# Kernel tuning notes

Measured on AMD Instinct MI355X. Metric: run time of the kernel, lower is better.

## Reference

```python
import jax, jax.numpy as jnp
import numpy as np

DIM = 512
HEADS = 8
HEAD_DIM = DIM // HEADS
SCALE = DIM ** (-0.5)  # source uses full dim, not head_dim
LAMBDA_COND = 1.0


def setup_inputs() -> dict:
    key = jax.random.key(0)
    ks = jax.random.split(key, 16)
    b, n, m_a, m_s = 4, 2048, 2048, 256
    s = 0.02
    inp = {
        "x": jax.random.normal(ks[0], (b, n, DIM), jnp.float32),
        "audio_context": jax.random.normal(ks[1], (b, m_a, DIM), jnp.float32),
        "singer_context": jax.random.normal(ks[2], (b, m_s, DIM), jnp.float32),
        "Wq": jax.random.normal(ks[3], (DIM, DIM), jnp.float32) * s,
        "bq": jnp.zeros((DIM,), jnp.float32),
        "Wka": jax.random.normal(ks[4], (DIM, DIM), jnp.float32) * s,
        "bka": jnp.zeros((DIM,), jnp.float32),
        "Wva": jax.random.normal(ks[5], (DIM, DIM), jnp.float32) * s,
        "bva": jnp.zeros((DIM,), jnp.float32),
        "Wks": jax.random.normal(ks[6], (DIM, DIM), jnp.float32) * s,
        "bks": jnp.zeros((DIM,), jnp.float32),
        "Wvs": jax.random.normal(ks[7], (DIM, DIM), jnp.float32) * s,
        "bvs": jnp.zeros((DIM,), jnp.float32),
        "Wp": jax.random.normal(ks[8], (DIM, DIM), jnp.float32) * s,
        "bp": jnp.zeros((DIM,), jnp.float32),
    }
    return inp


def _heads(t):
    b, n, c = t.shape
    return t.reshape(b, n, HEADS, HEAD_DIM).transpose(0, 2, 1, 3)  # (b,h,n,d)


def _attend(q, ctx, Wk, bk, Wv, bv):
    k = _heads(ctx @ Wk.T + bk)
    v = _heads(ctx @ Wv.T + bv)
    attn = jax.nn.softmax(jnp.einsum("bhnd,bhmd->bhnm", q, k) * SCALE, axis=-1)
    o = jnp.einsum("bhnm,bhmd->bhnd", attn, v)
    b, h, n, d = o.shape
    return o.transpose(0, 2, 1, 3).reshape(b, n, h * d)


def reference(x, audio_context, singer_context, Wq, bq, Wka, bka, Wva, bva,
              Wks, bks, Wvs, bvs, Wp, bp):
    q = _heads(x @ Wq.T + bq)
    x_audio = _attend(q, audio_context, Wka, bka, Wva, bva)
    x_singer = _attend(q, singer_context, Wks, bks, Wvs, bvs)
    out = x_audio + LAMBDA_COND * x_singer
    return out @ Wp.T + bp
```

## Files before the change

### kernel.cpp

```cpp
#include <hip/hip_runtime.h>

#define DIM 512
#define NQ 2048
#define MA 2048
#define MS 256
#define QSCALE 0.06375864651f

typedef __attribute__((ext_vector_type(8))) short bf16x8;
typedef __attribute__((ext_vector_type(4))) float f32x4;
typedef __attribute__((ext_vector_type(16))) float f32x16;

__device__ __forceinline__ ushort f2b(float f) {
    uint u = __float_as_uint(f);
    u = (u + 0x7fffu + ((u >> 16) & 1u)) >> 16;
    return (ushort)u;
}

__device__ __forceinline__ void gload16(const ushort* g, ushort* l) {
    __builtin_amdgcn_global_load_lds(
        (const __attribute__((address_space(1))) void*)g,
        (__attribute__((address_space(3))) void*)l, 16, 0, 0);
}

__global__ __launch_bounds__(256) void cast_all(const float* __restrict__ w0,
                                                const float* __restrict__ w1,
                                                const float* __restrict__ w2,
                                                const float* __restrict__ w3,
                                                const float* __restrict__ w4,
                                                const float* __restrict__ w5,
                                                const float* __restrict__ x,
                                                const float* __restrict__ ac,
                                                const float* __restrict__ scx,
                                                ushort* __restrict__ dst) {
    int i = blockIdx.x * 256 + threadIdx.x;
    const float* s;
    int o;
    if (i < 393216) {
        int w = i >> 16;
        s = w < 3 ? (w == 0 ? w0 : (w == 1 ? w1 : w2))
                  : (w == 3 ? w3 : (w == 4 ? w4 : w5));
        o = i & 65535;
    } else if (i < 1441792) { s = x;   o = i - 393216; }
    else if (i < 2490368)   { s = ac;  o = i - 1441792; }
    else                    { s = scx; o = i - 2490368; }
    float4 v = ((const float4*)s)[o];
    ushort4 u;
    u.x = f2b(v.x); u.y = f2b(v.y); u.z = f2b(v.z); u.w = f2b(v.w);
    ((ushort4*)dst)[i] = u;
}

struct GD {
    const ushort* A; const ushort* B; const float* bias; void* out;
    long sB, sO;
    int N, bx, by, blk0, biasrow, scaleq, outf32, pad;
};

__global__ __launch_bounds__(256) void gemm_fused(GD d0, GD d1, GD d2, GD d3, GD d4) {
    __shared__ ushort At[128 * 32];
    __shared__ ushort Bt[128 * 32];
    GD d = d0;
    int bid = blockIdx.x;
    if (bid >= d1.blk0) d = d1;
    if (bid >= d2.blk0) d = d2;
    if (bid >= d3.blk0) d = d3;
    if (bid >= d4.blk0) d = d4;
    int local = bid - d.blk0;
    int x = local % d.bx;
    int rem = local / d.bx;
    int y = rem % d.by;
    int z = rem / d.by;

    int t = threadIdx.x;
    int wv = t >> 6, ln = t & 63, l = ln & 15, g = ln >> 4;
    int wrow = wv & 1, wcol = wv >> 1;
    int row0 = x * 128, col0 = y * 128;
    int srow = t >> 2;
    int slot = (t & 3) * 8;
    int sko = ((t ^ srow) & 3) * 8;
    int kc8 = ((g ^ (l & 3)) & 3) * 8;
    const ushort* Ab = d.A;
    const ushort* Bb = d.B + (size_t)z * d.sB;
    int N = d.N;

    f32x4 acc[4][4];
#pragma unroll
    for (int i = 0; i < 4; i++)
#pragma unroll
        for (int j = 0; j < 4; j++) acc[i][j] = (f32x4){0, 0, 0, 0};

    for (int k0 = 0; k0 < 512; k0 += 32) {
        __syncthreads();
#pragma unroll
        for (int c = 0; c < 2; c++) {
            gload16(Ab + (size_t)(row0 + srow + 64 * c) * 512 + k0 + sko,
                    At + (srow + 64 * c) * 32 + slot);
            gload16(Bb + (size_t)(col0 + srow + 64 * c) * 512 + k0 + sko,
                    Bt + (srow + 64 * c) * 32 + slot);
        }
        __syncthreads();
        bf16x8 ar[4], br[4];
#pragma unroll
        for (int i = 0; i < 4; i++)
            ar[i] = *(const bf16x8*)(At + (wrow * 64 + i * 16 + l) * 32 + kc8);
#pragma unroll
        for (int j = 0; j < 4; j++)
            br[j] = *(const bf16x8*)(Bt + (wcol * 64 + j * 16 + l) * 32 + kc8);
#pragma unroll
        for (int i = 0; i < 4; i++)
#pragma unroll
            for (int j = 0; j < 4; j++)
                acc[i][j] = __builtin_amdgcn_mfma_f32_16x16x32_bf16(ar[i], br[j], acc[i][j], 0, 0, 0);
    }
#pragma unroll
    for (int i = 0; i < 4; i++) {
#pragma unroll
        for (int j = 0; j < 4; j++) {
            int row = row0 + wrow * 64 + i * 16 + g * 4;
            int col = col0 + wcol * 64 + j * 16 + l;
#pragma unroll
            for (int r = 0; r < 4; r++) {
                float bv = d.biasrow ? d.bias[row + r] : d.bias[col];
                float o = acc[i][j][r] + bv;
                if (d.scaleq) o *= QSCALE;
                if (d.outf32)
                    ((float*)d.out + (size_t)z * d.sO)[(size_t)(row + r) * N + col] = o;
                else
                    ((ushort*)d.out + (size_t)z * d.sO)[(size_t)(row + r) * N + col] = f2b(o);
            }
        }
    }
}

__device__ __forceinline__ void attn_ctx32(const ushort* __restrict__ kg,
                                           const ushort* __restrict__ vg,
                                           int M, const bf16x8 (&aq)[4],
                                           ushort* __restrict__ Kl,
                                           ushort* __restrict__ Vl,
                                           ushort* __restrict__ Pw,
                                           f32x16 (&o)[2], float& li,
                                           int l5, int hi, int sr, int sc) {
    bf16x8 k0 = *(const bf16x8*)kg;
    bf16x8 k1 = *(const bf16x8*)(kg + (size_t)32 * DIM);
    bf16x8 v0 = *(const bf16x8*)vg;
    bf16x8 v1 = *(const bf16x8*)(vg + (size_t)32 * M);
    for (int mt = 0; mt < M; mt += 64) {
        __syncthreads();
        *(bf16x8*)(Kl + sr * 72 + sc) = k0;
        *(bf16x8*)(Kl + (sr + 32) * 72 + sc) = k1;
        *(bf16x8*)(Vl + sr * 72 + sc) = v0;
        *(bf16x8*)(Vl + (sr + 32) * 72 + sc) = v1;
        __syncthreads();
        if (mt + 64 < M) {
            k0 = *(const bf16x8*)(kg + (size_t)(mt + 64) * DIM);
            k1 = *(const bf16x8*)(kg + (size_t)(mt + 96) * DIM);
            v0 = *(const bf16x8*)(vg + (mt + 64));
            v1 = *(const bf16x8*)(vg + (size_t)32 * M + (mt + 64));
        }
#pragma unroll
        for (int c = 0; c < 2; c++) {
            f32x16 s;
#pragma unroll
            for (int i = 0; i < 16; i++) s[i] = 0.f;
#pragma unroll
            for (int kd = 0; kd < 4; kd++) {
                bf16x8 kf = *(const bf16x8*)(Kl + (32 * c + l5) * 72 + kd * 16 + hi * 8);
                s = __builtin_amdgcn_mfma_f32_32x32x16_bf16(kf, aq[kd], s, 0, 0, 0);
            }
#pragma unroll
            for (int m = 0; m < 4; m++) {
                float p0 = exp2f(s[4 * m + 0]);
                float p1 = exp2f(s[4 * m + 1]);
                float p2 = exp2f(s[4 * m + 2]);
                float p3 = exp2f(s[4 * m + 3]);
                li += (p0 + p1) + (p2 + p3);
                uint2 pw;
                pw.x = ((__float_as_uint(p0) + 0x8000u) >> 16) |
                       ((__float_as_uint(p1) + 0x8000u) & 0xffff0000u);
                pw.y = ((__float_as_uint(p2) + 0x8000u) >> 16) |
                       ((__float_as_uint(p3) + 0x8000u) & 0xffff0000u);
                *(uint2*)(Pw + l5 * 72 + 32 * c + 8 * m + 4 * hi) = pw;
            }
        }
        bf16x8 pf[4];
#pragma unroll
        for (int kc = 0; kc < 4; kc++)
            pf[kc] = *(const bf16x8*)(Pw + l5 * 72 + kc * 16 + hi * 8);
#pragma unroll
        for (int dn = 0; dn < 2; dn++)
#pragma unroll
            for (int kc = 0; kc < 4; kc++) {
                bf16x8 vf = *(const bf16x8*)(Vl + (32 * dn + l5) * 72 + kc * 16 + hi * 8);
                o[dn] = __builtin_amdgcn_mfma_f32_32x32x16_bf16(pf[kc], vf, o[dn], 0, 0, 0);
            }
    }
}

__global__ __launch_bounds__(256) void attn_kernel(const ushort* __restrict__ q,
                                                   const ushort* __restrict__ Ka,
                                                   const ushort* __restrict__ VTa,
                                                   const ushort* __restrict__ Ks,
                                                   const ushort* __restrict__ VTs,
                                                   ushort* __restrict__ y) {
    __shared__ ushort Kl[64 * 72];
    __shared__ ushort Vl[64 * 72];
    __shared__ ushort Pl[4 * 32 * 72];
    int t = threadIdx.x;
    int wv = t >> 6, ln = t & 63, l5 = ln & 31, hi = ln >> 5;
    int h = blockIdx.y, bi = blockIdx.z;
    int q0 = blockIdx.x * 128 + wv * 32;
    bf16x8 aq[4];
    const ushort* qp = q + (size_t)(bi * NQ + q0 + l5) * DIM + h * 64 + hi * 8;
#pragma unroll
    for (int kd = 0; kd < 4; kd++) aq[kd] = *(const bf16x8*)(qp + kd * 16);
    int sr = t >> 3, sc = (t & 7) * 8;
    ushort* Pw = Pl + wv * 32 * 72;

    f32x16 o[2];
#pragma unroll
    for (int dn = 0; dn < 2; dn++)
#pragma unroll
        for (int i = 0; i < 16; i++) o[dn][i] = 0.f;
    float li = 0.f;

    attn_ctx32(Ks + (size_t)bi * MS * DIM + (size_t)sr * DIM + h * 64 + sc,
               VTs + (size_t)bi * DIM * MS + (size_t)(h * 64 + sr) * MS + sc,
               MS, aq, Kl, Vl, Pw, o, li, l5, hi, sr, sc);
    li += __shfl_xor(li, 32);
    float inv[16];
#pragma unroll
    for (int rg = 0; rg < 16; rg++)
        inv[rg] = 1.f / __shfl(li, (rg & 3) + 8 * (rg >> 2) + 4 * hi);
    float yv[2][16];
#pragma unroll
    for (int dn = 0; dn < 2; dn++)
#pragma unroll
        for (int rg = 0; rg < 16; rg++) yv[dn][rg] = o[dn][rg] * inv[rg];

#pragma unroll
    for (int dn = 0; dn < 2; dn++)
#pragma unroll
        for (int i = 0; i < 16; i++) o[dn][i] = 0.f;
    li = 0.f;
    attn_ctx32(Ka + (size_t)bi * MA * DIM + (size_t)sr * DIM + h * 64 + sc,
               VTa + (size_t)bi * DIM * MA + (size_t)(h * 64 + sr) * MA + sc,
               MA, aq, Kl, Vl, Pw, o, li, l5, hi, sr, sc);
    li += __shfl_xor(li, 32);
#pragma unroll
    for (int rg = 0; rg < 16; rg++)
        inv[rg] = 1.f / __shfl(li, (rg & 3) + 8 * (rg >> 2) + 4 * hi);

#pragma unroll
    for (int dn = 0; dn < 2; dn++)
#pragma unroll
        for (int rg = 0; rg < 16; rg++) {
            int qr = (rg & 3) + 8 * (rg >> 2) + 4 * hi;
            float ov = yv[dn][rg] + o[dn][rg] * inv[rg];
            y[(size_t)(bi * NQ + q0 + qr) * DIM + h * 64 + 32 * dn + l5] = f2b(ov);
        }
}

extern "C" void kernel_launch(void* const* d_in, const int* in_sizes, int n_in,
                              void* d_out, int out_size, void* d_ws, size_t ws_size,
                              hipStream_t stream) {
    const float* x   = (const float*)d_in[0];
    const float* ac  = (const float*)d_in[1];
    const float* scx = (const float*)d_in[2];
    const float* Wq  = (const float*)d_in[3];
    const float* bq  = (const float*)d_in[4];
    const float* Wka = (const float*)d_in[5];
    const float* bka = (const float*)d_in[6];
    const float* Wva = (const float*)d_in[7];
    const float* bva = (const float*)d_in[8];
    const float* Wks = (const float*)d_in[9];
    const float* bks = (const float*)d_in[10];
    const float* Wvs = (const float*)d_in[11];
    const float* bvs = (const float*)d_in[12];
    const float* Wp  = (const float*)d_in[13];
    const float* bp  = (const float*)d_in[14];

    ushort* wb   = (ushort*)d_ws;
    ushort* wqb  = wb;
    ushort* wkab = wb + 262144;
    ushort* wvab = wb + 2 * 262144;
    ushort* wksb = wb + 3 * 262144;
    ushort* wvsb = wb + 4 * 262144;
    ushort* wpb  = wb + 5 * 262144;
    ushort* xb   = wb + 6 * 262144;
    ushort* acb  = xb + 4194304;
    ushort* scxb = acb + 4194304;
    ushort* qb   = scxb + 524288;
    ushort* kab  = qb + 4194304;
    ushort* vta  = kab + 4194304;
    ushort* ksb  = vta + 4194304;
    ushort* vts  = ksb + 524288;
    ushort* yb   = xb;

    cast_all<<<10240, 256, 0, stream>>>(Wq, Wka, Wva, Wks, Wvs, Wp, x, ac, scx, wb);

    GD gq   = {xb,   wqb,  bq,  qb,  0, 0,               512,  64, 4,  0,   0, 1, 0, 0};
    GD gka  = {acb,  wkab, bka, kab, 0, 0,               512,  64, 4,  256, 0, 0, 0, 0};
    GD gvta = {wvab, acb,  bva, vta, 2048L * 512, 512L * 2048, 2048, 4, 16, 512, 1, 0, 0, 0};
    GD gks  = {scxb, wksb, bks, ksb, 0, 0,               512,  8,  4,  768, 0, 0, 0, 0};
    GD gvts = {wvsb, scxb, bvs, vts, 256L * 512, 512L * 256,   256,  4,  2,  800, 1, 0, 0, 0};
    gemm_fused<<<832, 256, 0, stream>>>(gq, gka, gvta, gks, gvts);

    attn_kernel<<<dim3(16, 8, 4), 256, 0, stream>>>(qb, kab, vta, ksb, vts, yb);

    GD gpr = {yb, wpb, bp, d_out, 0, 0, 512, 64, 4, 0, 0, 0, 1, 0};
    GD gnv = {nullptr, nullptr, nullptr, nullptr, 0, 0, 0, 1, 1, 1 << 30, 0, 0, 0, 0};
    gemm_fused<<<256, 256, 0, stream>>>(gpr, gnv, gnv, gnv, gnv);
}
```

Before: 252.8 us.

## Double-buffer K/V tiles and keep P in registers via permuted V layout

The attention inner loop now double-buffers K and V tiles in shared memory, so only one barrier per tile is needed and global loads are issued two tiles ahead. The softmax probabilities are packed straight into MFMA operand registers instead of making a round trip through a per-wave shared buffer. This works because V is stored with a permuted column order that matches the accumulator layout of the score MFMA. It also uses hardware exp2 and packed bf16 conversion builtins, which may change rounding slightly, and it doubles the K/V shared memory while dropping the P buffer.

```diff
diff --git a/kernel.cpp b/kernel.cpp
--- a/kernel.cpp
+++ b/kernel.cpp
@@ -14,6 +14,27 @@
     uint u = __float_as_uint(f);
     u = (u + 0x7fffu + ((u >> 16) & 1u)) >> 16;
     return (ushort)u;
+}
+
+__device__ __forceinline__ uint pk2bf(float a, float b) {
+#if __has_builtin(__builtin_amdgcn_cvt_pk_bf16_f32)
+    typedef __attribute__((ext_vector_type(2))) __bf16 bf2;
+    bf2 r = __builtin_amdgcn_cvt_pk_bf16_f32(a, b);
+    uint u;
+    __builtin_memcpy(&u, &r, 4);
+    return u;
+#else
+    return ((__float_as_uint(a) + 0x8000u) >> 16) |
+           ((__float_as_uint(b) + 0x8000u) & 0xffff0000u);
+#endif
+}
+
+__device__ __forceinline__ float fexp2(float x) {
+#if __has_builtin(__builtin_amdgcn_exp2f)
+    return __builtin_amdgcn_exp2f(x);
+#else
+    return exp2f(x);
+#endif
 }
 
 __device__ __forceinline__ void gload16(const ushort* g, ushort* l) {
@@ -136,62 +157,91 @@
                                            int M, const bf16x8 (&aq)[4],
                                            ushort* __restrict__ Kl,
                                            ushort* __restrict__ Vl,
-                                           ushort* __restrict__ Pw,
                                            f32x16 (&o)[2], float& li,
-                                           int l5, int hi, int sr, int sc) {
+                                           int l5, int hi, int sr, int sc, int vbase) {
+    int nt = M >> 6;
     bf16x8 k0 = *(const bf16x8*)kg;
     bf16x8 k1 = *(const bf16x8*)(kg + (size_t)32 * DIM);
     bf16x8 v0 = *(const bf16x8*)vg;
     bf16x8 v1 = *(const bf16x8*)(vg + (size_t)32 * M);
-    for (int mt = 0; mt < M; mt += 64) {
-        __syncthreads();
+    __syncthreads();
+    {
         *(bf16x8*)(Kl + sr * 72 + sc) = k0;
         *(bf16x8*)(Kl + (sr + 32) * 72 + sc) = k1;
-        *(bf16x8*)(Vl + sr * 72 + sc) = v0;
-        *(bf16x8*)(Vl + (sr + 32) * 72 + sc) = v1;
+        union { bf16x8 v; uint2 h[2]; } cv;
+        cv.v = v0;
+        *(uint2*)(Vl + sr * 72 + vbase) = cv.h[0];
+        *(uint2*)(Vl + sr * 72 + vbase + 8) = cv.h[1];
+        cv.v = v1;
+        *(uint2*)(Vl + (sr + 32) * 72 + vbase) = cv.h[0];
+        *(uint2*)(Vl + (sr + 32) * 72 + vbase + 8) = cv.h[1];
+    }
+    if (nt > 1) {
+        k0 = *(const bf16x8*)(kg + (size_t)64 * DIM);
+        k1 = *(const bf16x8*)(kg + (size_t)96 * DIM);
+        v0 = *(const bf16x8*)(vg + 64);
+        v1 = *(const bf16x8*)(vg + (size_t)32 * M + 64);
+    }
+    for (int i = 0; i < nt; i++) {
         __syncthreads();
-        if (mt + 64 < M) {
-            k0 = *(const bf16x8*)(kg + (size_t)(mt + 64) * DIM);
-            k1 = *(const bf16x8*)(kg + (size_t)(mt + 96) * DIM);
-            v0 = *(const bf16x8*)(vg + (mt + 64));
-            v1 = *(const bf16x8*)(vg + (size_t)32 * M + (mt + 64));
-        }
+        if (i + 1 < nt) {
+            ushort* Kb = Kl + ((i + 1) & 1) * (64 * 72);
+            ushort* Vb = Vl + ((i + 1) & 1) * (64 * 72);
+            *(bf16x8*)(Kb + sr * 72 + sc) = k0;
+            *(bf16x8*)(Kb + (sr + 32) * 72 + sc) = k1;
+            union { bf16x8 v; uint2 h[2]; } cv;
+            cv.v = v0;
+            *(uint2*)(Vb + sr * 72 + vbase) = cv.h[0];
+            *(uint2*)(Vb + sr * 72 + vbase + 8) = cv.h[1];
+            cv.v = v1;
+            *(uint2*)(Vb + (sr + 32) * 72 + vbase) = cv.h[0];
+            *(uint2*)(Vb + (sr + 32) * 72 + vbase + 8) = cv.h[1];
+        }
+        if (i + 2 < nt) {
+            size_t off = (size_t)(i + 2) * 64;
+            k0 = *(const bf16x8*)(kg + off * DIM);
+            k1 = *(const bf16x8*)(kg + (off + 32) * DIM);
+            v0 = *(const bf16x8*)(vg + off);
+            v1 = *(const bf16x8*)(vg + (size_t)32 * M + off);
+        }
+        const ushort* Kc = Kl + (i & 1) * (64 * 72);
+        const ushort* Vc = Vl + (i & 1) * (64 * 72);
+        uint2 pq[2][4];
 #pragma unroll
         for (int c = 0; c < 2; c++) {
+            bf16x8 kf[4];
+#pragma unroll
+            for (int kd = 0; kd < 4; kd++)
+                kf[kd] = *(const bf16x8*)(Kc + (32 * c + l5) * 72 + kd * 16 + hi * 8);
             f32x16 s;
 #pragma unroll
-            for (int i = 0; i < 16; i++) s[i] = 0.f;
-#pragma unroll
-            for (int kd = 0; kd < 4; kd++) {
-                bf16x8 kf = *(const bf16x8*)(Kl + (32 * c + l5) * 72 + kd * 16 + hi * 8);
-                s = __builtin_amdgcn_mfma_f32_32x32x16_bf16(kf, aq[kd], s, 0, 0, 0);
+            for (int ii = 0; ii < 16; ii++) s[ii] = 0.f;
+#pragma unroll
+            for (int kd = 0; kd < 4; kd++)
+                s = __builtin_amdgcn_mfma_f32_32x32x16_bf16(kf[kd], aq[kd], s, 0, 0, 0);
+#pragma unroll
+            for (int m = 0; m < 4; m++) {
+                float p0 = fexp2(s[4 * m + 0]);
+                float p1 = fexp2(s[4 * m + 1]);
+                float p2 = fexp2(s[4 * m + 2]);
+                float p3 = fexp2(s[4 * m + 3]);
+                li += (p0 + p1) + (p2 + p3);
+                pq[c][m].x = pk2bf(p0, p1);
+                pq[c][m].y = pk2bf(p2, p3);
             }
-#pragma unroll
-            for (int m = 0; m < 4; m++) {
-                float p0 = exp2f(s[4 * m + 0]);
-                float p1 = exp2f(s[4 * m + 1]);
-                float p2 = exp2f(s[4 * m + 2]);
-                float p3 = exp2f(s[4 * m + 3]);
-                li += (p0 + p1) + (p2 + p3);
-                uint2 pw;
-                pw.x = ((__float_as_uint(p0) + 0x8000u) >> 16) |
-                       ((__float_as_uint(p1) + 0x8000u) & 0xffff0000u);
-                pw.y = ((__float_as_uint(p2) + 0x8000u) >> 16) |
-                       ((__float_as_uint(p3) + 0x8000u) & 0xffff0000u);
-                *(uint2*)(Pw + l5 * 72 + 32 * c + 8 * m + 4 * hi) = pw;
+        }
+#pragma unroll
+        for (int kc = 0; kc < 4; kc++) {
+            int c = kc >> 1, m0 = 2 * (kc & 1);
+            union { bf16x8 v; uint u[4]; } w;
+            w.u[0] = pq[c][m0].x;     w.u[1] = pq[c][m0].y;
+            w.u[2] = pq[c][m0 + 1].x; w.u[3] = pq[c][m0 + 1].y;
+#pragma unroll
+            for (int dn = 0; dn < 2; dn++) {
+                bf16x8 vf = *(const bf16x8*)(Vc + (32 * dn + l5) * 72 + kc * 16 + hi * 8);
+                o[dn] = __builtin_amdgcn_mfma_f32_32x32x16_bf16(w.v, vf, o[dn], 0, 0, 0);
             }
         }
-        bf16x8 pf[4];
-#pragma unroll
-        for (int kc = 0; kc < 4; kc++)
-            pf[kc] = *(const bf16x8*)(Pw + l5 * 72 + kc * 16 + hi * 8);
-#pragma unroll
-        for (int dn = 0; dn < 2; dn++)
-#pragma unroll
-            for (int kc = 0; kc < 4; kc++) {
-                bf16x8 vf = *(const bf16x8*)(Vl + (32 * dn + l5) * 72 + kc * 16 + hi * 8);
-                o[dn] = __builtin_amdgcn_mfma_f32_32x32x16_bf16(pf[kc], vf, o[dn], 0, 0, 0);
-            }
     }
 }
 
@@ -201,9 +251,8 @@
                                                    const ushort* __restrict__ Ks,
                                                    const ushort* __restrict__ VTs,
                                                    ushort* __restrict__ y) {
-    __shared__ ushort Kl[64 * 72];
-    __shared__ ushort Vl[64 * 72];
-    __shared__ ushort Pl[4 * 32 * 72];
+    __shared__ ushort Kl[2 * 64 * 72];
+    __shared__ ushort Vl[2 * 64 * 72];
     int t = threadIdx.x;
     int wv = t >> 6, ln = t & 63, l5 = ln & 31, hi = ln >> 5;
     int h = blockIdx.y, bi = blockIdx.z;
@@ -213,7 +262,7 @@
 #pragma unroll
     for (int kd = 0; kd < 4; kd++) aq[kd] = *(const bf16x8*)(qp + kd * 16);
     int sr = t >> 3, sc = (t & 7) * 8;
-    ushort* Pw = Pl + wv * 32 * 72;
+    int vbase = (sc >> 4) * 16 + ((sc >> 3) & 1) * 4;
 
     f32x16 o[2];
 #pragma unroll
@@ -224,7 +273,7 @@
 
     attn_ctx32(Ks + (size_t)bi * MS * DIM + (size_t)sr * DIM + h * 64 + sc,
                VTs + (size_t)bi * DIM * MS + (size_t)(h * 64 + sr) * MS + sc,
-               MS, aq, Kl, Vl, Pw, o, li, l5, hi, sr, sc);
+               MS, aq, Kl, Vl, o, li, l5, hi, sr, sc, vbase);
     li += __shfl_xor(li, 32);
     float inv[16];
 #pragma unroll
@@ -243,7 +292,7 @@
     li = 0.f;
     attn_ctx32(Ka + (size_t)bi * MA * DIM + (size_t)sr * DIM + h * 64 + sc,
                VTa + (size_t)bi * DIM * MA + (size_t)(h * 64 + sr) * MA + sc,
-               MA, aq, Kl, Vl, Pw, o, li, l5, hi, sr, sc);
+               MA, aq, Kl, Vl, o, li, l5, hi, sr, sc, vbase);
     li += __shfl_xor(li, 32);
 #pragma unroll
     for (int rg = 0; rg < 16; rg++)
```

Result: faster. 227.0 us (-10.2%).
